# Kernel optimization log

Hardware: AMD Instinct MI355X
Metric: run time of the kernel (lower is better)

## Reference

```python
import jax, jax.numpy as jnp
import numpy as np

B, S, H, E, V, L = 64, 400, 512, 300, 50000, 1


def setup_inputs() -> dict:
    key = jax.random.key(0)
    ks = jax.random.split(key, 16)
    s = lambda k, shape, fan: jax.random.normal(k, shape, jnp.float32) * (1.0 / np.sqrt(fan))
    return {
        "x": jax.random.randint(ks[0], (B,), 0, V),
        "enc_out": jax.random.normal(ks[1], (B, S, H), jnp.float32),
        "h0": jax.random.normal(ks[2], (L, B, H), jnp.float32),
        "c0": jax.random.normal(ks[3], (L, B, H), jnp.float32),
        "text": jax.random.randint(ks[4], (B, S), 0, V),
        "batch_size": B,
        "emb_table": jax.random.normal(ks[5], (V, E), jnp.float32),
        "V_w": s(ks[6], (1, H), H),
        "V_b": jnp.zeros((1,), jnp.float32),
        "gen_w": s(ks[7], (1, 2 * H + E), 2 * H + E),
        "gen_b": jnp.zeros((1,), jnp.float32),
        "out_w": s(ks[8], (V, 2 * H), 2 * H),
        "out_b": jnp.zeros((V,), jnp.float32),
        "W_ih": s(ks[9], (4 * H, E + H), E + H),
        "W_hh": s(ks[10], (4 * H, H), H),
        "b_ih": jnp.zeros((4 * H,), jnp.float32),
        "b_hh": jnp.zeros((4 * H,), jnp.float32),
    }


def reference(x, enc_out, h0, c0, text, batch_size, emb_table, V_w, V_b,
              gen_w, gen_b, out_w, out_b, W_ih, W_hh, b_ih, b_hh):
    xe = emb_table[x]                                   # [B,E] (dropout off in eval)
    h_prev, c_prev = h0[0], c0[0]                       # [B,H], layers==1
    # Bahdanau attention: V(tanh(enc_out + dec_h)) softmaxed over seq
    score = jnp.tanh(enc_out + h_prev[:, None, :]) @ V_w.T + V_b   # [B,S,1]
    enc_weight = jax.nn.softmax(score, axis=1)                      # [B,S,1]
    ctx = jnp.sum(enc_weight * enc_out, axis=1)                     # [B,H]
    # single-step LSTM cell (torch gate order: i,f,g,o)
    d_in = jnp.concatenate([xe, ctx], axis=-1)                      # [B,E+H]
    gates = d_in @ W_ih.T + h_prev @ W_hh.T + b_ih + b_hh           # [B,4H]
    i, f, g, o = jnp.split(gates, 4, axis=-1)
    c_new = jax.nn.sigmoid(f) * c_prev + jax.nn.sigmoid(i) * jnp.tanh(g)
    h_new = jax.nn.sigmoid(o) * jnp.tanh(c_new)                     # [B,H]
    # pointer-generator combine
    out_cat = jnp.concatenate([h_new, ctx], axis=-1)                # [B,2H]
    gen_in = jnp.concatenate([ctx, h_new, xe], axis=-1)             # [B,2H+E]
    p_gen = jax.nn.sigmoid(gen_in @ gen_w.T + gen_b)[:, 0]          # [B]
    p_ptr = 1.0 - p_gen
    rows = jnp.arange(batch_size)[:, None]                          # [B,1]
    ptr_prob = jnp.zeros((batch_size, out_w.shape[0]), enc_out.dtype)
    ptr_prob = ptr_prob.at[rows, text].set(enc_weight[:, :, 0])     # scatter-set
    gen_prob = out_cat @ out_w.T + out_b                            # [B,V]
    out_prob = p_ptr[:, None] * ptr_prob + p_gen[:, None] * gen_prob
    return out_prob, h_new[None], c_new[None]
```

## Files before the change

kernel.cpp:

```cpp
#include <hip/hip_runtime.h>
#include <hip/hip_bf16.h>

#define BB 64
#define SS 400
#define HH 512
#define EE 300
#define VV 50000
#define KD 812
#define KG 1324
#define KC 1024
#define BV (BB*VV)

typedef __attribute__((ext_vector_type(8))) short bf16x8;
typedef __attribute__((ext_vector_type(4))) float f32x4;
typedef __attribute__((address_space(1))) const void gv_t;
typedef __attribute__((address_space(3))) void lv_t;

#define WS_SCORE 0
#define WS_W     25600
#define WS_CTX   51200
#define WS_HNEW  83968
#define WS_G0    116736
#define WS_G1    247808
#define WS_G2    378880
#define WS_G3    509952
#define WS_PGEN  641024
#define WS_PART  641088
#define WS_ABF   903232
#define WS_AD1   936000
#define WS_AD2   962624

__device__ __forceinline__ float sigm(float x){ return 1.f/(1.f+__expf(-x)); }
__device__ __forceinline__ float ftanh(float x){
  x = fminf(fmaxf(x,-15.f),15.f);
  float e = __expf(2.f*x);
  return (e-1.f)/(e+1.f);
}
__device__ __forceinline__ unsigned short f2bf(float f){
  unsigned int u = __builtin_bit_cast(unsigned int, f);
  u += 0x7fffu + ((u>>16)&1u);
  return (unsigned short)(u>>16);
}

#define LDW(S, off) { w##S##0 = *(const float4*)(wr + (off)*32); \
                      w##S##1 = *(const float4*)(wr + (off)*32 + 4); }
#define LDA(S, off) { a##S##0 = *(const bf16x8*)(a0 + (off)*32); \
                      a##S##1 = *(const bf16x8*)(a1 + (off)*32); \
                      a##S##2 = *(const bf16x8*)(a2 + (off)*32); \
                      a##S##3 = *(const bf16x8*)(a3 + (off)*32); }
#define CONS(S) { union { bf16x8 v; unsigned int u[4]; } bb_; \
  float4 f0_ = w##S##0; float4 f1_ = w##S##1; \
  asm("v_cvt_pk_bf16_f32 %0, %1, %2" : "=v"(bb_.u[0]) : "v"(f0_.x), "v"(f0_.y)); \
  asm("v_cvt_pk_bf16_f32 %0, %1, %2" : "=v"(bb_.u[1]) : "v"(f0_.z), "v"(f0_.w)); \
  asm("v_cvt_pk_bf16_f32 %0, %1, %2" : "=v"(bb_.u[2]) : "v"(f1_.x), "v"(f1_.y)); \
  asm("v_cvt_pk_bf16_f32 %0, %1, %2" : "=v"(bb_.u[3]) : "v"(f1_.z), "v"(f1_.w)); \
  acc0 = __builtin_amdgcn_mfma_f32_16x16x32_bf16(a##S##0, bb_.v, acc0, 0,0,0); \
  acc1 = __builtin_amdgcn_mfma_f32_16x16x32_bf16(a##S##1, bb_.v, acc1, 0,0,0); \
  acc2 = __builtin_amdgcn_mfma_f32_16x16x32_bf16(a##S##2, bb_.v, acc2, 0,0,0); \
  acc3 = __builtin_amdgcn_mfma_f32_16x16x32_bf16(a##S##3, bb_.v, acc3, 0,0,0); }

template<int NSTEP>
__device__ __forceinline__ void mfma_seg2(const float* __restrict__ wr,
    const unsigned short* __restrict__ a0, const unsigned short* __restrict__ a1,
    const unsigned short* __restrict__ a2, const unsigned short* __restrict__ a3,
    f32x4& acc0, f32x4& acc1, f32x4& acc2, f32x4& acc3)
{
  static_assert(NSTEP % 2 == 0 && NSTEP >= 4, "");
  float4 wA0,wA1, wB0,wB1;
  bf16x8 aA0,aA1,aA2,aA3, aB0,aB1,aB2,aB3;
  LDW(A,0) LDA(A,0)
  LDW(B,1) LDA(B,1)
  #pragma unroll
  for (int ks=0; ks<NSTEP; ks+=2){
    CONS(A) if (ks+2 < NSTEP){ LDW(A,ks+2) LDA(A,ks+2) }
    CONS(B) if (ks+3 < NSTEP){ LDW(B,ks+3) LDA(B,ks+3) }
  }
}

__global__ __launch_bounds__(256) void k_prep(const int* __restrict__ x,
    const float* __restrict__ emb, const float* __restrict__ h0,
    unsigned short* __restrict__ ad1, unsigned short* __restrict__ ad2)
{
  int n = blockIdx.x*256 + threadIdx.x;
  if (n < BB*832){
    int b = n/832, k = n - b*832;
    if (k < EE) ad1[n] = f2bf(emb[(size_t)x[b]*EE + k]);
    else if (k >= 812) ad1[n] = 0;
  } else {
    int m = n - BB*832;
    ad2[m] = f2bf(h0[m]);
  }
}

__global__ __launch_bounds__(256) void k_score(const float* __restrict__ enc,
    const float* __restrict__ h0, const float* __restrict__ Vw,
    const float* __restrict__ Vb, float* __restrict__ score)
{
  int wv = threadIdx.x >> 6, lane = threadIdx.x & 63;
  int pair = blockIdx.x*4 + wv;
  int b = pair / SS;
  int i0 = lane*8;
  const float4* ep = (const float4*)(enc + (size_t)pair*HH + i0);
  const float4* hp = (const float4*)(h0 + b*HH + i0);
  const float4* vp = (const float4*)(Vw + i0);
  float4 e0 = ep[0], e1 = ep[1];
  float4 hv0 = hp[0], hv1 = hp[1];
  float4 v0 = vp[0], v1 = vp[1];
  float sum = ftanh(e0.x+hv0.x)*v0.x + ftanh(e0.y+hv0.y)*v0.y
            + ftanh(e0.z+hv0.z)*v0.z + ftanh(e0.w+hv0.w)*v0.w
            + ftanh(e1.x+hv1.x)*v1.x + ftanh(e1.y+hv1.y)*v1.y
            + ftanh(e1.z+hv1.z)*v1.z + ftanh(e1.w+hv1.w)*v1.w;
  #pragma unroll
  for (int off=32; off; off>>=1) sum += __shfl_xor(sum, off);
  if (lane==0) score[pair] = sum + Vb[0];
}

__global__ __launch_bounds__(256) void k_ctx(const float* __restrict__ enc,
    const float* __restrict__ score, float* __restrict__ wout,
    float* __restrict__ part)
{
  __shared__ float red[256];
  __shared__ float wl[SS];
  int b = blockIdx.x >> 3, sp = blockIdx.x & 7;
  int t = threadIdx.x;
  float v1 = score[b*SS + t];
  float v2 = (t < SS-256) ? score[b*SS + t + 256] : -1e30f;
  red[t] = fmaxf(v1, v2);
  __syncthreads();
  for (int o=128; o; o>>=1){ if (t<o) red[t] = fmaxf(red[t], red[t+o]); __syncthreads(); }
  float mx = red[0];
  __syncthreads();
  float e1 = __expf(v1 - mx);
  float e2 = (t < SS-256) ? __expf(v2 - mx) : 0.f;
  red[t] = e1 + e2;
  __syncthreads();
  for (int o=128; o; o>>=1){ if (t<o) red[t] += red[t+o]; __syncthreads(); }
  float inv = 1.f/red[0];
  float w1 = e1*inv;
  wl[t] = w1;
  if (sp==0) wout[b*SS + t] = w1;
  if (t < SS-256){
    float w2 = e2*inv;
    wl[t+256] = w2;
    if (sp==0) wout[b*SS + t + 256] = w2;
  }
  __syncthreads();
  float a0 = 0.f, a1 = 0.f;
  const float* ebase = enc + ((size_t)b*SS + sp*50)*HH + 2*t;
  #pragma unroll 5
  for (int s=0; s<50; ++s){
    float wg = wl[sp*50 + s];
    float2 e = *(const float2*)(ebase + s*HH);
    a0 += wg * e.x;
    a1 += wg * e.y;
  }
  *(float2*)(part + (size_t)(b*8+sp)*HH + 2*t) = make_float2(a0, a1);
}

__global__ __launch_bounds__(256) void k_ctx_reduce(const float* __restrict__ part,
    float* __restrict__ ctx, unsigned short* __restrict__ ad1)
{
  int b = blockIdx.x, t = threadIdx.x;
  float a0=0.f, a1=0.f;
  #pragma unroll
  for (int sp=0; sp<8; ++sp){
    float2 e = *(const float2*)(part + (size_t)(b*8+sp)*HH + 2*t);
    a0 += e.x; a1 += e.y;
  }
  *(float2*)(ctx + b*HH + 2*t) = make_float2(a0, a1);
  ad1[b*832 + EE + 2*t]     = f2bf(a0);
  ad1[b*832 + EE + 2*t + 1] = f2bf(a1);
}

__global__ __launch_bounds__(128, 4) void k_gates(const float* __restrict__ Wih,
    const float* __restrict__ Whh, const unsigned short* __restrict__ ad1,
    const unsigned short* __restrict__ ad2,
    float* __restrict__ g0, float* __restrict__ g1,
    float* __restrict__ g2, float* __restrict__ g3)
{
  int wt = blockIdx.x*2 + (threadIdx.x >> 6);
  int lane = threadIdx.x & 63;
  int col = lane & 15, kg = lane >> 4;
  int jt = wt >> 2, part = wt & 3;
  int j = jt*16 + col;
  f32x4 acc0={0.f,0.f,0.f,0.f}, acc1=acc0, acc2=acc0, acc3=acc0;
  float* g;
  if (part < 2){
    int k0 = part ? 384 : 0;
    const float* wr = Wih + (size_t)j*KD + k0 + kg*8;
    const unsigned short* a = ad1 + col*832 + k0 + kg*8;
    if (part) mfma_seg2<14>(wr, a, a+16*832, a+32*832, a+48*832, acc0,acc1,acc2,acc3);
    else      mfma_seg2<12>(wr, a, a+16*832, a+32*832, a+48*832, acc0,acc1,acc2,acc3);
    g = part ? g1 : g0;
  } else {
    int k0 = (part==3) ? 256 : 0;
    const float* wr = Whh + (size_t)j*HH + k0 + kg*8;
    const unsigned short* a = ad2 + col*512 + k0 + kg*8;
    mfma_seg2<8>(wr, a, a+16*512, a+32*512, a+48*512, acc0,acc1,acc2,acc3);
    g = (part==3) ? g3 : g2;
  }
  #pragma unroll
  for (int i=0;i<4;i++){
    g[(size_t)j*BB + 0*16 + kg*4 + i] = acc0[i];
    g[(size_t)j*BB + 1*16 + kg*4 + i] = acc1[i];
    g[(size_t)j*BB + 2*16 + kg*4 + i] = acc2[i];
    g[(size_t)j*BB + 3*16 + kg*4 + i] = acc3[i];
  }
}

__global__ __launch_bounds__(256) void k_lstm(const float* __restrict__ c0,
    const float* __restrict__ bih, const float* __restrict__ bhh,
    const float* __restrict__ g0, const float* __restrict__ g1,
    const float* __restrict__ g2, const float* __restrict__ g3,
    const float* __restrict__ ctx, float* __restrict__ hnew,
    unsigned short* __restrict__ abf, float* __restrict__ out)
{
  int n = blockIdx.x*256 + threadIdx.x;
  int b = n & 63, h = n >> 6;
  #define GSUM(off) (g0[(off)*BB+b] + g1[(off)*BB+b] + g2[(off)*BB+b] + g3[(off)*BB+b] + bih[off] + bhh[off])
  float gi = GSUM(h);
  float gf = GSUM(HH+h);
  float gg = GSUM(2*HH+h);
  float go = GSUM(3*HH+h);
  #undef GSUM
  float cn = sigm(gf)*c0[b*HH+h] + sigm(gi)*ftanh(gg);
  float hn = sigm(go)*ftanh(cn);
  out[BV + b*HH + h]          = hn;
  out[BV + BB*HH + b*HH + h]  = cn;
  hnew[b*HH + h] = hn;
  abf[b*KC + h]      = f2bf(hn);
  abf[b*KC + HH + h] = f2bf(ctx[b*HH + h]);
}

__global__ __launch_bounds__(256) void k_pgen(const float* __restrict__ genw,
    const float* __restrict__ genb, const float* __restrict__ ctx,
    const float* __restrict__ hnew, const int* __restrict__ x,
    const float* __restrict__ emb, float* __restrict__ pgen)
{
  __shared__ float red[256];
  int b = blockIdx.x, t = threadIdx.x;
  float p = 0.f;
  for (int k=t; k<KG; k+=256){
    float g = genw[k];
    float v = (k < HH) ? ctx[b*HH + k]
            : (k < 2*HH) ? hnew[b*HH + k - HH]
            : emb[(size_t)x[b]*EE + (k - 2*HH)];
    p += g*v;
  }
  red[t] = p; __syncthreads();
  for (int o=128; o; o>>=1){ if (t<o) red[t] += red[t+o]; __syncthreads(); }
  if (t==0) pgen[b] = sigm(red[0] + genb[0]);
}

#define PADB 4112
__global__ __launch_bounds__(512, 2) void k_gemm(const float* __restrict__ out_w,
    const float* __restrict__ out_b, const unsigned short* __restrict__ abf,
    const float* __restrict__ pgen, float* __restrict__ out)
{
  __shared__ __align__(16) char wlds[2][16*PADB];
  __shared__ float comb[4][16][17];
  int t = threadIdx.x;
  int w = t >> 6, lane = t & 63;
  int col = lane & 15, kg = lane >> 4;
  int mt = w >> 1, kh = w & 1;
  int bid = blockIdx.x;
  int ts = (bid * 3125) >> 8;
  int te = ((bid + 1) * 3125) >> 8;

  const unsigned short* ap = abf + (size_t)(mt*16 + col)*KC + kh*512 + kg*8;
  bf16x8 pa[16];
  #pragma unroll
  for (int ks=0; ks<16; ++ks) pa[ks] = *(const bf16x8*)(ap + ks*32);

  #define DMASTAGE(buf_, tile_) { \
    const char* wb_ = (const char*)(out_w + (size_t)(tile_)*16*KC); \
    _Pragma("unroll") \
    for (int i_=0;i_<8;i_++){ \
      int c_ = w*8 + i_; \
      int r_ = c_ >> 2, q_ = c_ & 3; \
      __builtin_amdgcn_global_load_lds( \
        (gv_t*)(wb_ + r_*4096 + q_*1024 + lane*16), \
        (lv_t*)(&wlds[buf_][0] + r_*PADB + q_*1024), 16, 0, 0); \
    } }

  DMASTAGE(0, ts)
  int cur = 0;
  for (int tile = ts; tile < te; ++tile){
    __syncthreads();
    if (tile + 1 < te) DMASTAGE(cur^1, tile+1)

    const char* rb = &wlds[cur][0] + col*PADB + kh*2048 + kg*32;
    f32x4 acc = {0.f,0.f,0.f,0.f};
    #pragma unroll
    for (int ks=0; ks<16; ++ks){
      float4 f0 = *(const float4*)(rb + ks*128);
      float4 f1 = *(const float4*)(rb + ks*128 + 16);
      union { bf16x8 v; unsigned int u[4]; } bb;
      asm("v_cvt_pk_bf16_f32 %0, %1, %2" : "=v"(bb.u[0]) : "v"(f0.x), "v"(f0.y));
      asm("v_cvt_pk_bf16_f32 %0, %1, %2" : "=v"(bb.u[1]) : "v"(f0.z), "v"(f0.w));
      asm("v_cvt_pk_bf16_f32 %0, %1, %2" : "=v"(bb.u[2]) : "v"(f1.x), "v"(f1.y));
      asm("v_cvt_pk_bf16_f32 %0, %1, %2" : "=v"(bb.u[3]) : "v"(f1.z), "v"(f1.w));
      acc = __builtin_amdgcn_mfma_f32_16x16x32_bf16(pa[ks], bb.v, acc, 0,0,0);
    }

    if (kh == 1){
      #pragma unroll
      for (int i=0;i<4;i++) comb[mt][kg*4 + i][col] = acc[i];
    }
    asm volatile("s_waitcnt lgkmcnt(0)");
    __builtin_amdgcn_sched_barrier(0);
    __builtin_amdgcn_s_barrier();
    __builtin_amdgcn_sched_barrier(0);
    if (kh == 0){
      int v = tile*16 + col;
      float ob = out_b[v];
      #pragma unroll
      for (int i=0;i<4;i++){
        int b = mt*16 + kg*4 + i;
        out[(size_t)b*VV + v] = pgen[b]*(acc[i] + comb[mt][kg*4 + i][col] + ob);
      }
    }
    cur ^= 1;
  }
  #undef DMASTAGE
}

__global__ __launch_bounds__(256) void k_scatter(const int* __restrict__ text,
    const float* __restrict__ w, const float* __restrict__ pgen,
    float* __restrict__ out)
{
  __shared__ int ts[SS];
  int b = blockIdx.x, t = threadIdx.x;
  ts[t] = text[b*SS + t];
  if (t + 256 < SS) ts[t+256] = text[b*SS + t + 256];
  __syncthreads();
  float pp = 1.f - pgen[b];
  #pragma unroll
  for (int rep=0; rep<2; ++rep){
    int s = t + rep*256;
    if (s < SS){
      int v = ts[s];
      bool dup = false;
      #pragma unroll 4
      for (int s2=s+1; s2<SS; ++s2) dup = dup || (ts[s2]==v);
      if (!dup) out[(size_t)b*VV + v] += pp * w[b*SS + s];
    }
  }
}

extern "C" void kernel_launch(void* const* d_in, const int* in_sizes, int n_in,
                              void* d_out, int out_size, void* d_ws, size_t ws_size,
                              hipStream_t stream)
{
  const int*   x    = (const int*)  d_in[0];
  const float* enc  = (const float*)d_in[1];
  const float* h0   = (const float*)d_in[2];
  const float* c0   = (const float*)d_in[3];
  const int*   text = (const int*)  d_in[4];
  const float* emb  = (const float*)d_in[6];
  const float* Vw   = (const float*)d_in[7];
  const float* Vb   = (const float*)d_in[8];
  const float* genw = (const float*)d_in[9];
  const float* genb = (const float*)d_in[10];
  const float* outw = (const float*)d_in[11];
  const float* outb = (const float*)d_in[12];
  const float* Wih  = (const float*)d_in[13];
  const float* Whh  = (const float*)d_in[14];
  const float* bih  = (const float*)d_in[15];
  const float* bhh  = (const float*)d_in[16];
  float* out = (float*)d_out;

  float* ws     = (float*)d_ws;
  float* score  = ws + WS_SCORE;
  float* wbuf   = ws + WS_W;
  float* ctx    = ws + WS_CTX;
  float* hnew   = ws + WS_HNEW;
  float* g0     = ws + WS_G0;
  float* g1     = ws + WS_G1;
  float* g2     = ws + WS_G2;
  float* g3     = ws + WS_G3;
  float* pgen   = ws + WS_PGEN;
  float* part   = ws + WS_PART;
  unsigned short* abf = (unsigned short*)(ws + WS_ABF);
  unsigned short* ad1 = (unsigned short*)(ws + WS_AD1);
  unsigned short* ad2 = (unsigned short*)(ws + WS_AD2);

  k_prep<<<336, 256, 0, stream>>>(x, emb, h0, ad1, ad2);
  k_score<<<6400, 256, 0, stream>>>(enc, h0, Vw, Vb, score);
  k_ctx<<<512, 256, 0, stream>>>(enc, score, wbuf, part);
  k_ctx_reduce<<<64, 256, 0, stream>>>(part, ctx, ad1);
  k_gates<<<256, 128, 0, stream>>>(Wih, Whh, ad1, ad2, g0, g1, g2, g3);
  k_lstm<<<128, 256, 0, stream>>>(c0, bih, bhh, g0, g1, g2, g3, ctx, hnew, abf, out);
  k_pgen<<<64, 256, 0, stream>>>(genw, genb, ctx, hnew, x, emb, pgen);
  k_gemm<<<256, 512, 0, stream>>>(outw, outb, abf, pgen, out);
  k_scatter<<<64, 256, 0, stream>>>(text, wbuf, pgen, out);
}
```

Measured before the change: 129.3 us.

## Split output GEMM K into two half-stages per block and drop cross-wave reduction

The vocabulary GEMM now uses 256-thread blocks where each wave owns all of K for one 16-row M tile. It streams each weight tile in two K-halves through the double-buffered LDS, which halves the LDS footprint per stage. This removes the LDS partial-sum exchange and extra barrier between K-split waves. The grid doubles to 512 blocks. Each wave now holds twice as many A-fragment registers and there are two barriers per tile, which could hurt occupancy or latency hiding.

```diff
diff --git a/kernel.cpp b/kernel.cpp
--- a/kernel.cpp
+++ b/kernel.cpp
@@ -252,77 +252,79 @@
   if (t==0) pgen[b] = sigm(red[0] + genb[0]);
 }
 
-#define PADB 4112
-__global__ __launch_bounds__(512, 2) void k_gemm(const float* __restrict__ out_w,
+#define ROWB 4096
+#define HROWB 2048
+#define PADH 2064
+__global__ __launch_bounds__(256, 2) void k_gemm(const float* __restrict__ out_w,
     const float* __restrict__ out_b, const unsigned short* __restrict__ abf,
     const float* __restrict__ pgen, float* __restrict__ out)
 {
-  __shared__ __align__(16) char wlds[2][16*PADB];
-  __shared__ float comb[4][16][17];
+  __shared__ __align__(16) char wlds[2][16*PADH];
   int t = threadIdx.x;
   int w = t >> 6, lane = t & 63;
   int col = lane & 15, kg = lane >> 4;
-  int mt = w >> 1, kh = w & 1;
   int bid = blockIdx.x;
-  int ts = (bid * 3125) >> 8;
-  int te = ((bid + 1) * 3125) >> 8;
-
-  const unsigned short* ap = abf + (size_t)(mt*16 + col)*KC + kh*512 + kg*8;
-  bf16x8 pa[16];
-  #pragma unroll
-  for (int ks=0; ks<16; ++ks) pa[ks] = *(const bf16x8*)(ap + ks*32);
-
-  #define DMASTAGE(buf_, tile_) { \
-    const char* wb_ = (const char*)(out_w + (size_t)(tile_)*16*KC); \
+  int ts = (bid * 3125) >> 9;
+  int te = ((bid + 1) * 3125) >> 9;
+
+  const unsigned short* ap = abf + (size_t)(w*16 + col)*KC + kg*8;
+  bf16x8 pa0[16], pa1[16];
+  #pragma unroll
+  for (int ks=0; ks<16; ++ks){
+    pa0[ks] = *(const bf16x8*)(ap + ks*32);
+    pa1[ks] = *(const bf16x8*)(ap + 512 + ks*32);
+  }
+
+  #define DMASTEP(buf_, tile_, kh_) { \
+    const char* wb_ = (const char*)out_w + (size_t)(tile_)*16*ROWB + (kh_)*HROWB; \
     _Pragma("unroll") \
     for (int i_=0;i_<8;i_++){ \
       int c_ = w*8 + i_; \
-      int r_ = c_ >> 2, q_ = c_ & 3; \
+      int r_ = c_ >> 1, q_ = c_ & 1; \
       __builtin_amdgcn_global_load_lds( \
-        (gv_t*)(wb_ + r_*4096 + q_*1024 + lane*16), \
-        (lv_t*)(&wlds[buf_][0] + r_*PADB + q_*1024), 16, 0, 0); \
+        (gv_t*)(wb_ + (size_t)r_*ROWB + q_*1024 + lane*16), \
+        (lv_t*)(&wlds[buf_][0] + r_*PADH + q_*1024), 16, 0, 0); \
     } }
 
-  DMASTAGE(0, ts)
+  #define HALFCOMPUTE(buf_, PA_) { \
+    const char* rb_ = &wlds[buf_][0] + col*PADH + kg*32; \
+    _Pragma("unroll") \
+    for (int ks=0; ks<16; ++ks){ \
+      float4 f0 = *(const float4*)(rb_ + ks*128); \
+      float4 f1 = *(const float4*)(rb_ + ks*128 + 16); \
+      union { bf16x8 v; unsigned int u[4]; } bb; \
+      asm("v_cvt_pk_bf16_f32 %0, %1, %2" : "=v"(bb.u[0]) : "v"(f0.x), "v"(f0.y)); \
+      asm("v_cvt_pk_bf16_f32 %0, %1, %2" : "=v"(bb.u[1]) : "v"(f0.z), "v"(f0.w)); \
+      asm("v_cvt_pk_bf16_f32 %0, %1, %2" : "=v"(bb.u[2]) : "v"(f1.x), "v"(f1.y)); \
+      asm("v_cvt_pk_bf16_f32 %0, %1, %2" : "=v"(bb.u[3]) : "v"(f1.z), "v"(f1.w)); \
+      acc = __builtin_amdgcn_mfma_f32_16x16x32_bf16(PA_[ks], bb.v, acc, 0,0,0); \
+    } }
+
+  DMASTEP(0, ts, 0)
   int cur = 0;
   for (int tile = ts; tile < te; ++tile){
+    f32x4 acc = {0.f,0.f,0.f,0.f};
+
     __syncthreads();
-    if (tile + 1 < te) DMASTAGE(cur^1, tile+1)
-
-    const char* rb = &wlds[cur][0] + col*PADB + kh*2048 + kg*32;
-    f32x4 acc = {0.f,0.f,0.f,0.f};
+    DMASTEP(cur^1, tile, 1)
+    HALFCOMPUTE(cur, pa0)
+    cur ^= 1;
+
+    __syncthreads();
+    if (tile + 1 < te) DMASTEP(cur^1, tile+1, 0)
+    HALFCOMPUTE(cur, pa1)
+    cur ^= 1;
+
+    int v = tile*16 + col;
+    float ob = out_b[v];
     #pragma unroll
-    for (int ks=0; ks<16; ++ks){
-      float4 f0 = *(const float4*)(rb + ks*128);
-      float4 f1 = *(const float4*)(rb + ks*128 + 16);
-      union { bf16x8 v; unsigned int u[4]; } bb;
-      asm("v_cvt_pk_bf16_f32 %0, %1, %2" : "=v"(bb.u[0]) : "v"(f0.x), "v"(f0.y));
-      asm("v_cvt_pk_bf16_f32 %0, %1, %2" : "=v"(bb.u[1]) : "v"(f0.z), "v"(f0.w));
-      asm("v_cvt_pk_bf16_f32 %0, %1, %2" : "=v"(bb.u[2]) : "v"(f1.x), "v"(f1.y));
-      asm("v_cvt_pk_bf16_f32 %0, %1, %2" : "=v"(bb.u[3]) : "v"(f1.z), "v"(f1.w));
-      acc = __builtin_amdgcn_mfma_f32_16x16x32_bf16(pa[ks], bb.v, acc, 0,0,0);
+    for (int i=0;i<4;i++){
+      int b = w*16 + kg*4 + i;
+      out[(size_t)b*VV + v] = pgen[b]*(acc[i] + ob);
     }
-
-    if (kh == 1){
-      #pragma unroll
-      for (int i=0;i<4;i++) comb[mt][kg*4 + i][col] = acc[i];
-    }
-    asm volatile("s_waitcnt lgkmcnt(0)");
-    __builtin_amdgcn_sched_barrier(0);
-    __builtin_amdgcn_s_barrier();
-    __builtin_amdgcn_sched_barrier(0);
-    if (kh == 0){
-      int v = tile*16 + col;
-      float ob = out_b[v];
-      #pragma unroll
-      for (int i=0;i<4;i++){
-        int b = mt*16 + kg*4 + i;
-        out[(size_t)b*VV + v] = pgen[b]*(acc[i] + comb[mt][kg*4 + i][col] + ob);
-      }
-    }
-    cur ^= 1;
-  }
-  #undef DMASTAGE
+  }
+  #undef DMASTEP
+  #undef HALFCOMPUTE
 }
 
 __global__ __launch_bounds__(256) void k_scatter(const int* __restrict__ text,
@@ -392,6 +394,6 @@
   k_gates<<<256, 128, 0, stream>>>(Wih, Whh, ad1, ad2, g0, g1, g2, g3);
   k_lstm<<<128, 256, 0, stream>>>(c0, bih, bhh, g0, g1, g2, g3, ctx, hnew, abf, out);
   k_pgen<<<64, 256, 0, stream>>>(genw, genb, ctx, hnew, x, emb, pgen);
-  k_gemm<<<256, 512, 0, stream>>>(outw, outb, abf, pgen, out);
+  k_gemm<<<512, 256, 0, stream>>>(outw, outb, abf, pgen, out);
   k_scatter<<<64, 256, 0, stream>>>(text, wbuf, pgen, out);
 }
```

Result: faster. 126.1 us (-2.4%).
